# Kernel tuning notes

Measured on AMD Instinct MI355X. Metric: run time of the kernel, lower is better.

Reference implementation:

```python
import jax, jax.numpy as jnp
import numpy as np

FACTOR = 50
IN_CHANNELS = 512

def setup_inputs() -> dict:
    key = jax.random.key(0)
    ks = jax.random.split(key, 9)
    B, Cin, W, H = 16, 256, 64, 64
    D = 512  # out_channels
    L = W * H
    U = FACTOR * int(np.ceil(np.log(L)))  # 450
    return {
        "input_1": jax.random.normal(ks[0], (B, Cin, W, H), jnp.float32),
        "input_2": jax.random.normal(ks[1], (B, Cin, W, H), jnp.float32),
        "Wq": jax.random.normal(ks[2], (D, 2 * Cin), jnp.float32) * 0.02,
        "bq": jax.random.normal(ks[3], (D,), jnp.float32) * 0.02,
        "Wk": jax.random.normal(ks[4], (D, 2 * Cin), jnp.float32) * 0.02,
        "bk": jax.random.normal(ks[5], (D,), jnp.float32) * 0.02,
        "Wv": jax.random.normal(ks[6], (D, 2 * Cin), jnp.float32) * 0.02,
        "bv": jax.random.normal(ks[7], (D,), jnp.float32) * 0.02,
        "idx_sample": jax.random.randint(ks[8], (U,), 0, L, jnp.int32),
    }

def reference(input_1, input_2, Wq, bq, Wk, bk, Wv, bv, idx_sample):
    x = jnp.concatenate([input_1, input_2], axis=1)  # [B, 2*Cin, W, H]
    B, C, Wd, Ht = x.shape
    L = Wd * Ht
    D = Wq.shape[0]
    # 1x1 convs == per-pixel channel matmul; then torch's raw .view to [B,1,L,D]
    def proj(Wm, bm):
        y = jnp.einsum('bchw,oc->bohw', x, Wm) + bm[None, :, None, None]
        return y.reshape(B, 1, L, D)  # memory reinterpretation, as in torch .view
    q = proj(Wq, bq)
    k = proj(Wk, bk)
    v = proj(Wv, bv)

    u = min(FACTOR * int(np.ceil(np.log(L))), L)  # n_top == sample_k here
    # sampled Q-K scores
    K_sample = k[:, :, idx_sample, :]                      # [B,1,U,D]
    QKs = jnp.einsum('bhld,bhsd->bhls', q, K_sample)       # [B,1,L,U]
    M = QKs.max(-1) - QKs.sum(-1) / L                      # sparsity measure [B,1,L]
    M_top = jax.lax.top_k(M, u)[1]                         # [B,1,u]
    Q_reduce = jnp.take_along_axis(q, M_top[..., None], axis=2)  # [B,1,u,D]
    scores = jnp.einsum('bhud,bhld->bhul', Q_reduce, k)    # [B,1,u,L]
    scores = scores * (1.0 / IN_CHANNELS ** 0.5)

    # initial context: mean of V broadcast over queries
    context = jnp.broadcast_to(v.mean(axis=2, keepdims=True), (B, 1, L, D))
    attn = jax.nn.softmax(scores, axis=-1)                 # [B,1,u,L]
    upd = jnp.einsum('bhul,bhld->bhud', attn, v)           # [B,1,u,D]
    bI = jnp.arange(B)[:, None, None]
    hI = jnp.arange(1)[None, :, None]
    context = context.at[bI, hI, M_top].set(upd)
    # transpose(2,1) then torch .view to [B, D, W, H]
    out = context.transpose(0, 2, 1, 3).reshape(B, D, Wd, Ht)
    return out
```

## Files before the change

kernel.cpp:

```cpp
#include <hip/hip_runtime.h>
#include <cstdint>
#include <cstddef>

#define L_DIM 4096
#define D_DIM 512
#define CIN   256
#define BATCH 16
#define KSPLIT 4

typedef _Float16 half8 __attribute__((ext_vector_type(8)));
typedef unsigned short ushort8 __attribute__((ext_vector_type(8)));
typedef float f32x4 __attribute__((ext_vector_type(4)));

__device__ __forceinline__ void gld16(const _Float16* g, _Float16* l) {
    __builtin_amdgcn_global_load_lds(
        (const __attribute__((address_space(1))) unsigned int*)g,
        (__attribute__((address_space(3))) unsigned int*)l,
        16, 0, 0);
}

__global__ __launch_bounds__(256) void convert_w(
    const float* __restrict__ Wq, const float* __restrict__ Wk,
    const float* __restrict__ Wv,
    _Float16* __restrict__ Wh, _Float16* __restrict__ Wl)
{
    const int w = blockIdx.y;
    const float* src = (w == 0) ? Wq : (w == 1) ? Wk : Wv;
    int i = blockIdx.x * 256 + threadIdx.x;
    float xv = src[i];
    _Float16 hi = (_Float16)xv;
    Wh[(size_t)w * 262144 + i] = hi;
    Wl[(size_t)w * 262144 + i] = (_Float16)(xv - (float)hi);
}

__global__ __launch_bounds__(256) void convert_x(
    const float* __restrict__ x1, const float* __restrict__ x2,
    _Float16* __restrict__ XTh, _Float16* __restrict__ XTl, int phase)
{
    const int bb = blockIdx.z;
    const int b = phase * 8 + bb;
    const int s0 = blockIdx.x * 64;
    const int c0 = blockIdx.y * 64;
    __shared__ float t[64][65];
    const int tid = threadIdx.x;
    const int g = tid >> 6, sy = tid & 63;
    const float* src = (c0 < CIN)
        ? (x1 + (size_t)b * CIN * L_DIM + (size_t)c0 * L_DIM)
        : (x2 + (size_t)b * CIN * L_DIM + (size_t)(c0 - CIN) * L_DIM);
    #pragma unroll
    for (int r = 0; r < 16; r++) {
        int cl = g * 16 + r;
        t[cl][sy] = src[(size_t)cl * L_DIM + s0 + sy];
    }
    __syncthreads();
    _Float16* outh = XTh + (size_t)bb * L_DIM * 512 + (size_t)s0 * 512 + c0;
    _Float16* outl = XTl + (size_t)bb * L_DIM * 512 + (size_t)s0 * 512 + c0;
    #pragma unroll
    for (int r = 0; r < 16; r++) {
        int sl = g * 16 + r;
        float xv = t[sy][sl];
        _Float16 hi = (_Float16)xv;
        float lo = xv - (float)hi;
        outh[(size_t)sl * 512 + sy] = hi;
        outl[(size_t)sl * 512 + sy] = (_Float16)lo;
    }
}

__global__ __launch_bounds__(256) void proj_mfma(
    const _Float16* __restrict__ Wh, const _Float16* __restrict__ Wl,
    const _Float16* __restrict__ XTh, const _Float16* __restrict__ XTl,
    const float* __restrict__ bq, const float* __restrict__ bk,
    const float* __restrict__ bv,
    _Float16* __restrict__ qh, _Float16* __restrict__ ql,
    _Float16* __restrict__ kh, _Float16* __restrict__ kl,
    _Float16* __restrict__ vh,
    int phase)
{
    const int z = blockIdx.z;
    const int bb = z / 3, w = z % 3;
    const int b = phase * 8 + bb;
    const _Float16* Ah_g = Wh + (size_t)w * 262144;
    const _Float16* Al_g = Wl + (size_t)w * 262144;
    const _Float16* Bh_g = XTh + (size_t)bb * ((size_t)L_DIM * 512);
    const _Float16* Bl_g = XTl + (size_t)bb * ((size_t)L_DIM * 512);
    const float* bias = (w == 0) ? bq : (w == 1) ? bk : bv;
    _Float16* outh = ((w == 0) ? qh : (w == 1) ? kh : vh) + (size_t)b * ((size_t)D_DIM * L_DIM);
    _Float16* outl = ((w == 0) ? ql : (w == 1) ? kl : (_Float16*)0);
    if (outl) outl += (size_t)b * ((size_t)D_DIM * L_DIM);

    const int m0 = blockIdx.y * 128;
    const int n0 = blockIdx.x * 128;

    __shared__ _Float16 lds[4 * 128 * 32];
    _Float16* ldsA_h = lds;
    _Float16* ldsA_l = lds + 4096;
    _Float16* ldsB_h = lds + 8192;
    _Float16* ldsB_l = lds + 12288;

    const int tid = threadIdx.x;
    const int w4 = tid >> 6, lane = tid & 63;
    const int lr = lane & 15, quad = lane >> 4;
    const int wr = w4 >> 1, wc = w4 & 1;

    f32x4 acc[4][4] = {};

    const int q1 = w4 * 128 + lane, q2 = q1 + 64;
    const int r1 = q1 >> 2, c41 = q1 & 3;
    const int r2 = q2 >> 2, c42 = q2 & 3;

    const _Float16* pAh1 = Ah_g + (size_t)(m0 + r1) * 512 + c41 * 8;
    const _Float16* pAh2 = Ah_g + (size_t)(m0 + r2) * 512 + c42 * 8;
    const _Float16* pAl1 = Al_g + (size_t)(m0 + r1) * 512 + c41 * 8;
    const _Float16* pAl2 = Al_g + (size_t)(m0 + r2) * 512 + c42 * 8;
    const _Float16* pBh1 = Bh_g + (size_t)(n0 + r1) * 512 + c41 * 8;
    const _Float16* pBh2 = Bh_g + (size_t)(n0 + r2) * 512 + c42 * 8;
    const _Float16* pBl1 = Bl_g + (size_t)(n0 + r1) * 512 + c41 * 8;
    const _Float16* pBl2 = Bl_g + (size_t)(n0 + r2) * 512 + c42 * 8;

    _Float16* d1 = (_Float16*)(lds) + (size_t)(w4 * 128) * 8;
    _Float16* d2 = (_Float16*)(lds) + (size_t)(w4 * 128 + 64) * 8;

    for (int k0 = 0; k0 < 512; k0 += 32) {
        if (k0) __syncthreads();
        gld16(pAh1 + k0, d1);
        gld16(pAh2 + k0, d2);
        gld16(pAl1 + k0, d1 + 4096);
        gld16(pAl2 + k0, d2 + 4096);
        gld16(pBh1 + k0, d1 + 8192);
        gld16(pBh2 + k0, d2 + 8192);
        gld16(pBl1 + k0, d1 + 12288);
        gld16(pBl2 + k0, d2 + 12288);
        __syncthreads();

        half8 fAh[4], fAl[4];
        #pragma unroll
        for (int i = 0; i < 4; i++) {
            int m = wr * 64 + i * 16 + lr;
            fAh[i] = *(const half8*)(ldsA_h + m * 32 + quad * 8);
            fAl[i] = *(const half8*)(ldsA_l + m * 32 + quad * 8);
        }
        #pragma unroll
        for (int j = 0; j < 4; j++) {
            int n = wc * 64 + j * 16 + lr;
            half8 fBh = *(const half8*)(ldsB_h + n * 32 + quad * 8);
            half8 fBl = *(const half8*)(ldsB_l + n * 32 + quad * 8);
            #pragma unroll
            for (int i = 0; i < 4; i++) {
                acc[i][j] = __builtin_amdgcn_mfma_f32_16x16x32_f16(fAh[i], fBh, acc[i][j], 0, 0, 0);
                acc[i][j] = __builtin_amdgcn_mfma_f32_16x16x32_f16(fAl[i], fBh, acc[i][j], 0, 0, 0);
                acc[i][j] = __builtin_amdgcn_mfma_f32_16x16x32_f16(fAh[i], fBl, acc[i][j], 0, 0, 0);
            }
        }
    }

    #pragma unroll
    for (int i = 0; i < 4; i++) {
        int mg = m0 + wr * 64 + i * 16 + quad * 4;
        #pragma unroll
        for (int r = 0; r < 4; r++) {
            float bvv = bias[mg + r];
            #pragma unroll
            for (int j = 0; j < 4; j++) {
                int ng = n0 + wc * 64 + j * 16 + lr;
                float val = acc[i][j][r] + bvv;
                _Float16 hi = (_Float16)val;
                size_t off = (size_t)(mg + r) * L_DIM + ng;
                outh[off] = hi;
                if (w != 2) outl[off] = (_Float16)(val - (float)hi);
            }
        }
    }
}

__global__ __launch_bounds__(256) void qks_mfma(
    const _Float16* __restrict__ qh, const _Float16* __restrict__ ql,
    const _Float16* __restrict__ kh, const _Float16* __restrict__ kl,
    const int* __restrict__ idx_sample,
    float* __restrict__ Mmax, float* __restrict__ Msum, int U, int nst)
{
    const int b = blockIdx.z;
    const int stile = blockIdx.y;
    const int l0 = blockIdx.x * 128;
    const int s0 = stile * 128;
    const size_t perB = (size_t)D_DIM * L_DIM;
    const _Float16* qh_b = qh + (size_t)b * perB;
    const _Float16* ql_b = ql + (size_t)b * perB;
    const _Float16* kh_b = kh + (size_t)b * perB;
    const _Float16* kl_b = kl + (size_t)b * perB;

    __shared__ _Float16 ldsAh[4096], ldsAl[4096];
    __shared__ _Float16 ldsBh[4096], ldsBl[4096];
    __shared__ int sidx[128];
    __shared__ float redm[8][128];
    __shared__ float reds[8][128];

    const int tid = threadIdx.x;
    const int w4 = tid >> 6, lane = tid & 63;
    const int lr = lane & 15, quad = lane >> 4;
    const int ws = w4 >> 1, wl = w4 & 1;

    if (tid < 128) {
        int s = s0 + tid;
        sidx[tid] = (s < U) ? idx_sample[s] : idx_sample[0];
    }
    __syncthreads();

    f32x4 acc[4][4] = {};

    for (int k0 = 0; k0 < 512; k0 += 32) {
        #pragma unroll
        for (int t = 0; t < 2; t++) {
            int c = w4 * 128 + t * 64 + lane;
            int row = c >> 2, part = c & 3;
            int krow = sidx[row];
            size_t go = (size_t)krow * 512 + k0 + part * 8;
            size_t qo = (size_t)(l0 + row) * 512 + k0 + part * 8;
            int base = (w4 * 128 + t * 64) * 8;
            gld16(kh_b + go, ldsAh + base);
            gld16(kl_b + go, ldsAl + base);
            gld16(qh_b + qo, ldsBh + base);
            gld16(ql_b + qo, ldsBl + base);
        }
        __syncthreads();

        half8 fAh[4], fAl[4];
        #pragma unroll
        for (int i = 0; i < 4; i++) {
            int s = ws * 64 + i * 16 + lr;
            fAh[i] = *(const half8*)(ldsAh + s * 32 + quad * 8);
            fAl[i] = *(const half8*)(ldsAl + s * 32 + quad * 8);
        }
        #pragma unroll
        for (int j = 0; j < 4; j++) {
            int l = wl * 64 + j * 16 + lr;
            half8 fBh = *(const half8*)(ldsBh + l * 32 + quad * 8);
            half8 fBl = *(const half8*)(ldsBl + l * 32 + quad * 8);
            #pragma unroll
            for (int i = 0; i < 4; i++) {
                acc[i][j] = __builtin_amdgcn_mfma_f32_16x16x32_f16(fAh[i], fBh, acc[i][j], 0, 0, 0);
                acc[i][j] = __builtin_amdgcn_mfma_f32_16x16x32_f16(fAl[i], fBh, acc[i][j], 0, 0, 0);
                acc[i][j] = __builtin_amdgcn_mfma_f32_16x16x32_f16(fAh[i], fBl, acc[i][j], 0, 0, 0);
            }
        }
        __syncthreads();
    }

    float runmax[4], runsum[4];
    #pragma unroll
    for (int j = 0; j < 4; j++) { runmax[j] = -__builtin_inff(); runsum[j] = 0.f; }
    #pragma unroll
    for (int i = 0; i < 4; i++) {
        #pragma unroll
        for (int r = 0; r < 4; r++) {
            int sg = s0 + ws * 64 + i * 16 + quad * 4 + r;
            if (sg < U) {
                #pragma unroll
                for (int j = 0; j < 4; j++) {
                    runmax[j] = fmaxf(runmax[j], acc[i][j][r]);
                    runsum[j] += acc[i][j][r];
                }
            }
        }
    }
    #pragma unroll
    for (int j = 0; j < 4; j++) {
        int l = wl * 64 + j * 16 + lr;
        redm[ws * 4 + quad][l] = runmax[j];
        reds[ws * 4 + quad][l] = runsum[j];
    }
    __syncthreads();
    if (tid < 128) {
        float gm = -__builtin_inff(), gs = 0.f;
        #pragma unroll
        for (int t = 0; t < 8; t++) { gm = fmaxf(gm, redm[t][tid]); gs += reds[t][tid]; }
        size_t o = ((size_t)b * nst + stile) * L_DIM + l0 + tid;
        Mmax[o] = gm;
        Msum[o] = gs;
    }
}

__global__ __launch_bounds__(512) void topk_select(
    const float* __restrict__ Mmax, const float* __restrict__ Msum,
    int* __restrict__ topidx, int U, int nst)
{
    const int b = blockIdx.x;
    const int tid = threadIdx.x;
    __shared__ int wcnt[8];
    __shared__ int basec;

    unsigned mykey[8];
    #pragma unroll
    for (int t = 0; t < 8; t++) {
        int l = t * 512 + tid;
        float gm = -__builtin_inff(), gs = 0.f;
        for (int st = 0; st < nst; st++) {
            size_t o = ((size_t)b * nst + st) * L_DIM + l;
            gm = fmaxf(gm, Mmax[o]);
            gs += Msum[o];
        }
        float M = gm - gs * (1.f / (float)L_DIM);
        unsigned bits = __float_as_uint(M);
        mykey[t] = (bits & 0x80000000u) ? ~bits : (bits | 0x80000000u);
    }
    if (tid == 0) basec = 0;

    const int wv = tid >> 6, lane = tid & 63;
    unsigned lo = 0u, hi = 0xFFFFFFFFu;
    while (lo < hi) {
        unsigned hl = hi - lo;
        unsigned mid = lo + (hl >> 1) + (hl & 1u);
        int c = 0;
        #pragma unroll
        for (int t = 0; t < 8; t++) c += (mykey[t] >= mid) ? 1 : 0;
        #pragma unroll
        for (int o = 32; o > 0; o >>= 1) c += __shfl_down(c, o, 64);
        if (lane == 0) wcnt[wv] = c;
        __syncthreads();
        int total = 0;
        #pragma unroll
        for (int i = 0; i < 8; i++) total += wcnt[i];
        if (total >= U) lo = mid; else hi = mid - 1;
        __syncthreads();
    }
    #pragma unroll
    for (int t = 0; t < 8; t++) {
        if (mykey[t] >= lo) {
            int pos = atomicAdd(&basec, 1);
            if (pos < U) topidx[b * U + pos] = t * 512 + tid;
        }
    }
}

__global__ __launch_bounds__(512) void vmean_partial(
    const _Float16* __restrict__ vh, float* __restrict__ partial)
{
    const int ch = blockIdx.x, b = blockIdx.y;
    const int d = threadIdx.x;
    const _Float16* vhb = vh + (size_t)b * ((size_t)D_DIM * L_DIM);
    float acc = 0.f;
    const int lbeg = ch * 128;
    for (int l = lbeg; l < lbeg + 128; l++)
        acc += (float)vhb[(size_t)l * D_DIM + d];
    partial[((size_t)b * 32 + ch) * D_DIM + d] = acc;
}

__global__ __launch_bounds__(512) void vmean_reduce(const float* __restrict__ partial,
                                                    float* __restrict__ vmean)
{
    const int b = blockIdx.x;
    const int d = threadIdx.x;
    float acc = 0.f;
    for (int ch = 0; ch < 32; ch++) acc += partial[((size_t)b * 32 + ch) * D_DIM + d];
    vmean[b * D_DIM + d] = acc * (1.f / (float)L_DIM);
}

__global__ __launch_bounds__(256) void fill_out(const float* __restrict__ vmean,
                                                float* __restrict__ out)
{
    const int z = blockIdx.x;
    const int b = z >> 6, lch = z & 63;
    __shared__ float vm[512];
    vm[threadIdx.x] = vmean[b * 512 + threadIdx.x];
    vm[threadIdx.x + 256] = vmean[b * 512 + threadIdx.x + 256];
    __syncthreads();
    float* op = out + (size_t)b * ((size_t)D_DIM * L_DIM) + (size_t)lch * 64 * 512;
    #pragma unroll
    for (int it = 0; it < 32; it++) {
        int flat = (threadIdx.x + it * 256) * 4;
        int d = flat & 511;
        float4 r = { vm[d], vm[d + 1], vm[d + 2], vm[d + 3] };
        *(float4*)&op[flat] = r;
    }
}

__global__ __launch_bounds__(256) void zero_sel(const int* __restrict__ topidx,
                                                float* __restrict__ out, int U)
{
    const int u = blockIdx.x, b = blockIdx.y;
    int row = topidx[b * U + u];
    float2 z = { 0.f, 0.f };
    *(float2*)&out[(size_t)b * ((size_t)D_DIM * L_DIM) + (size_t)row * 512
                   + threadIdx.x * 2] = z;
}

__global__ __launch_bounds__(256) void scores_mfma(
    const _Float16* __restrict__ qh, const _Float16* __restrict__ kh,
    const int* __restrict__ topidx,
    _Float16* __restrict__ sh, int U)
{
    const int b = blockIdx.z;
    const int s0 = blockIdx.x * 128;
    const int u0 = blockIdx.y * 128;
    const size_t perB = (size_t)D_DIM * L_DIM;
    const _Float16* qh_b = qh + (size_t)b * perB;
    const _Float16* kh_b = kh + (size_t)b * perB;
    _Float16* sh_b = sh + (size_t)b * (size_t)U * L_DIM;

    __shared__ _Float16 ldsAh[4096];
    __shared__ _Float16 ldsBh[4096];
    __shared__ int arow[128];

    const int tid = threadIdx.x;
    const int w4 = tid >> 6, lane = tid & 63;
    const int lr = lane & 15, quad = lane >> 4;
    const int wu = w4 >> 1, wn = w4 & 1;

    if (tid < 128) {
        int u = u0 + tid;
        arow[tid] = topidx[b * U + (u < U ? u : U - 1)];
    }
    __syncthreads();

    f32x4 acc[4][4] = {};

    for (int k0 = 0; k0 < 512; k0 += 32) {
        #pragma unroll
        for (int t = 0; t < 2; t++) {
            int c = w4 * 128 + t * 64 + lane;
            int row = c >> 2, part = c & 3;
            size_t go = (size_t)arow[row] * 512 + k0 + part * 8;
            size_t ko = (size_t)(s0 + row) * 512 + k0 + part * 8;
            int base = (w4 * 128 + t * 64) * 8;
            gld16(qh_b + go, ldsAh + base);
            gld16(kh_b + ko, ldsBh + base);
        }
        __syncthreads();

        half8 fAh[4];
        #pragma unroll
        for (int i = 0; i < 4; i++) {
            int u = wu * 64 + i * 16 + lr;
            fAh[i] = *(const half8*)(ldsAh + u * 32 + quad * 8);
        }
        #pragma unroll
        for (int j = 0; j < 4; j++) {
            int s = wn * 64 + j * 16 + lr;
            half8 fBh = *(const half8*)(ldsBh + s * 32 + quad * 8);
            #pragma unroll
            for (int i = 0; i < 4; i++)
                acc[i][j] = __builtin_amdgcn_mfma_f32_16x16x32_f16(fAh[i], fBh, acc[i][j], 0, 0, 0);
        }
        __syncthreads();
    }

    const float scale = 0.044194173824159216f;
    #pragma unroll
    for (int i = 0; i < 4; i++) {
        #pragma unroll
        for (int r = 0; r < 4; r++) {
            int u = u0 + wu * 64 + i * 16 + quad * 4 + r;
            if (u < U) {
                #pragma unroll
                for (int j = 0; j < 4; j++) {
                    int s = s0 + wn * 64 + j * 16 + lr;
                    sh_b[(size_t)u * L_DIM + s] = (_Float16)(acc[i][j][r] * scale);
                }
            }
        }
    }
}

__global__ __launch_bounds__(256) void softmax_h(_Float16* __restrict__ sh)
{
    _Float16* hrow = sh + (size_t)blockIdx.x * L_DIM;
    const int tid = threadIdx.x;
    float x[16];
    #pragma unroll
    for (int t = 0; t < 2; t++) {
        half8 h8 = *(const half8*)(hrow + tid * 8 + t * 2048);
        #pragma unroll
        for (int i = 0; i < 8; i++) x[t * 8 + i] = (float)h8[i];
    }
    __shared__ float red[256];
    float lm = -__builtin_inff();
    #pragma unroll
    for (int i = 0; i < 16; i++) lm = fmaxf(lm, x[i]);
    red[tid] = lm;
    __syncthreads();
    for (int o = 128; o > 0; o >>= 1) {
        if (tid < o) red[tid] = fmaxf(red[tid], red[tid + o]);
        __syncthreads();
    }
    float m = red[0];
    __syncthreads();
    float ls = 0.f;
    #pragma unroll
    for (int i = 0; i < 16; i++) { x[i] = __expf(x[i] - m); ls += x[i]; }
    red[tid] = ls;
    __syncthreads();
    for (int o = 128; o > 0; o >>= 1) {
        if (tid < o) red[tid] += red[tid + o];
        __syncthreads();
    }
    float inv = 1.f / red[0];
    #pragma unroll
    for (int t = 0; t < 2; t++) {
        half8 h8;
        #pragma unroll
        for (int i = 0; i < 8; i++) h8[i] = (_Float16)(x[t * 8 + i] * inv);
        *(half8*)(hrow + tid * 8 + t * 2048) = h8;
    }
}

__global__ __launch_bounds__(256) void upd_mfma(
    const _Float16* __restrict__ sh, const _Float16* __restrict__ vh,
    const int* __restrict__ topidx, float* __restrict__ out, int U)
{
    const int zz = blockIdx.z;
    const int b = zz >> 2, ks = zz & 3;
    const int n0 = blockIdx.y * 128;
    const int u0 = blockIdx.x * 128;
    const size_t perB = (size_t)D_DIM * L_DIM;
    const _Float16* ah_b = sh + (size_t)b * (size_t)U * L_DIM;
    const _Float16* vh_b = vh + (size_t)b * perB;

    __shared__ _Float16 ldsAh[4096];
    __shared__ _Float16 ldsBh[4096];

    const int tid = threadIdx.x;
    const int w4 = tid >> 6, lane = tid & 63;
    const int lr = lane & 15, quad = lane >> 4;
    const int wu = w4 >> 1, wd = w4 & 1;

    const int part = tid & 15, spair = tid >> 4;
    const int s_b = spair * 2;
    const int colw = ((spair >> 2) + part) & 3;
    const int so2 = (s_b & 7);

    f32x4 acc[4][4] = {};

    const int kbeg = ks * (L_DIM / KSPLIT);
    const int kend = kbeg + (L_DIM / KSPLIT);
    for (int k0 = kbeg; k0 < kend; k0 += 32) {
        #pragma unroll
        for (int t = 0; t < 2; t++) {
            int c = w4 * 128 + t * 64 + lane;
            int u = c >> 2, pt = c & 3;
            int urow = u0 + u; if (urow >= U) urow = U - 1;
            size_t ao = (size_t)urow * L_DIM + k0 + pt * 8;
            int base = (w4 * 128 + t * 64) * 8;
            gld16(ah_b + ao, ldsAh + base);
        }
        {
            const _Float16* s0p = vh_b + (size_t)(k0 + s_b) * 512 + n0 + part * 8;
            const _Float16* s1p = s0p + 512;
            ushort8 a0 = *(const ushort8*)s0p;
            ushort8 a1 = *(const ushort8*)s1p;
            #pragma unroll
            for (int t = 0; t < 8; t++) {
                int dd = part * 8 + t;
                unsigned int ph = (unsigned int)a0[t] | ((unsigned int)a1[t] << 16);
                *(unsigned int*)(ldsBh + dd * 32 + colw * 8 + so2) = ph;
            }
        }
        __syncthreads();

        half8 fAh[4];
        #pragma unroll
        for (int i = 0; i < 4; i++) {
            int u = wu * 64 + i * 16 + lr;
            fAh[i] = *(const half8*)(ldsAh + u * 32 + quad * 8);
        }
        #pragma unroll
        for (int j = 0; j < 4; j++) {
            int dd = wd * 64 + j * 16 + lr;
            int col = (quad + (dd >> 3)) & 3;
            half8 fBh = *(const half8*)(ldsBh + dd * 32 + col * 8);
            #pragma unroll
            for (int i = 0; i < 4; i++)
                acc[i][j] = __builtin_amdgcn_mfma_f32_16x16x32_f16(fAh[i], fBh, acc[i][j], 0, 0, 0);
        }
        __syncthreads();
    }

    #pragma unroll
    for (int i = 0; i < 4; i++) {
        #pragma unroll
        for (int r = 0; r < 4; r++) {
            int u = u0 + wu * 64 + i * 16 + quad * 4 + r;
            if (u < U) {
                int lrow = topidx[b * U + u];
                #pragma unroll
                for (int j = 0; j < 4; j++) {
                    int dd = n0 + wd * 64 + j * 16 + lr;
                    unsafeAtomicAdd(&out[(size_t)b * perB + (size_t)lrow * 512 + dd],
                                    acc[i][j][r]);
                }
            }
        }
    }
}

extern "C" void kernel_launch(void* const* d_in, const int* in_sizes, int n_in,
                              void* d_out, int out_size, void* d_ws, size_t ws_size,
                              hipStream_t stream)
{
    const float* x1 = (const float*)d_in[0];
    const float* x2 = (const float*)d_in[1];
    const float* Wq = (const float*)d_in[2];
    const float* bq = (const float*)d_in[3];
    const float* Wk = (const float*)d_in[4];
    const float* bk = (const float*)d_in[5];
    const float* Wv = (const float*)d_in[6];
    const float* bv = (const float*)d_in[7];
    const int*  idx = (const int*)d_in[8];
    const int U = in_sizes[8];
    const int nst = (U + 127) / 128;

    float* out = (float*)d_out;

    const size_t perB = (size_t)D_DIM * L_DIM;
    const size_t tenH = (size_t)BATCH * perB;
    _Float16* qh = (_Float16*)d_ws;
    _Float16* ql = qh + tenH;
    _Float16* kh = ql + tenH;
    _Float16* kl = kh + tenH;
    _Float16* vh = kl + tenH;
    float* S = (float*)(vh + tenH);

    _Float16* XTh = (_Float16*)S;
    _Float16* XTl = XTh + (size_t)8 * L_DIM * 512;
    _Float16* Wh  = XTl + (size_t)8 * L_DIM * 512;
    _Float16* Wl  = Wh + (size_t)3 * 512 * 512;

    _Float16* sh = (_Float16*)S;
    float* vmean = (float*)(sh + (size_t)BATCH * (size_t)U * L_DIM);
    float* partU = vmean + (size_t)BATCH * D_DIM;
    float* vpart = partU;
    float* Mmax  = partU;
    float* Msum  = Mmax + (size_t)BATCH * nst * L_DIM;
    int* topidx  = (int*)(partU + (size_t)2 * BATCH * 4 * L_DIM);

    convert_w<<<dim3(1024, 3), 256, 0, stream>>>(Wq, Wk, Wv, Wh, Wl);

    for (int phase = 0; phase < 2; phase++) {
        convert_x<<<dim3(64, 8, 8), 256, 0, stream>>>(x1, x2, XTh, XTl, phase);
        proj_mfma<<<dim3(L_DIM / 128, D_DIM / 128, 8 * 3), 256, 0, stream>>>(
            Wh, Wl, XTh, XTl, bq, bk, bv, qh, ql, kh, kl, vh, phase);
    }

    vmean_partial<<<dim3(32, BATCH), 512, 0, stream>>>(vh, vpart);
    vmean_reduce<<<BATCH, 512, 0, stream>>>(vpart, vmean);
    fill_out<<<BATCH * 64, 256, 0, stream>>>(vmean, out);

    qks_mfma<<<dim3(L_DIM / 128, nst, BATCH), 256, 0, stream>>>(
        qh, ql, kh, kl, idx, Mmax, Msum, U, nst);
    topk_select<<<BATCH, 512, 0, stream>>>(Mmax, Msum, topidx, U, nst);

    const int utiles = (U + 127) / 128;
    scores_mfma<<<dim3(L_DIM / 128, utiles, BATCH), 256, 0, stream>>>(
        qh, kh, topidx, sh, U);
    softmax_h<<<BATCH * U, 256, 0, stream>>>(sh);
    zero_sel<<<dim3(U, BATCH), 256, 0, stream>>>(topidx, out, U);
    upd_mfma<<<dim3(utiles, D_DIM / 128, BATCH * KSPLIT), 256, 0, stream>>>(
        sh, vh, topidx, out, U);
}
```

Before: 915.6 us.

## Swizzle LDS tiles to avoid bank conflicts and split V projection to single-precision path

Applies an XOR swizzle to the 16-byte column chunks in LDS across the projection, QK-sample, scores and update GEMMs, so that MFMA fragment reads from 64-byte rows no longer hit the same banks. It also splits the V projection into its own kernel that skips the low-half (Wl, XTl) operand loads and the two correction MFMAs, since V is stored only in fp16 high. The V kernel therefore uses half the LDS and a third of the MFMAs. In exchange there is one more kernel launch per phase, and V is now computed with less precision than before because the W and X low-half corrections are dropped.

```diff
diff --git a/kernel.cpp b/kernel.cpp
--- a/kernel.cpp
+++ b/kernel.cpp
@@ -66,27 +66,24 @@
     }
 }
 
-__global__ __launch_bounds__(256) void proj_mfma(
+__global__ __launch_bounds__(256) void proj_mfma_qk(
     const _Float16* __restrict__ Wh, const _Float16* __restrict__ Wl,
     const _Float16* __restrict__ XTh, const _Float16* __restrict__ XTl,
     const float* __restrict__ bq, const float* __restrict__ bk,
-    const float* __restrict__ bv,
     _Float16* __restrict__ qh, _Float16* __restrict__ ql,
     _Float16* __restrict__ kh, _Float16* __restrict__ kl,
-    _Float16* __restrict__ vh,
     int phase)
 {
     const int z = blockIdx.z;
-    const int bb = z / 3, w = z % 3;
+    const int bb = z >> 1, w = z & 1;
     const int b = phase * 8 + bb;
     const _Float16* Ah_g = Wh + (size_t)w * 262144;
     const _Float16* Al_g = Wl + (size_t)w * 262144;
     const _Float16* Bh_g = XTh + (size_t)bb * ((size_t)L_DIM * 512);
     const _Float16* Bl_g = XTl + (size_t)bb * ((size_t)L_DIM * 512);
-    const float* bias = (w == 0) ? bq : (w == 1) ? bk : bv;
-    _Float16* outh = ((w == 0) ? qh : (w == 1) ? kh : vh) + (size_t)b * ((size_t)D_DIM * L_DIM);
-    _Float16* outl = ((w == 0) ? ql : (w == 1) ? kl : (_Float16*)0);
-    if (outl) outl += (size_t)b * ((size_t)D_DIM * L_DIM);
+    const float* bias = (w == 0) ? bq : bk;
+    _Float16* outh = ((w == 0) ? qh : kh) + (size_t)b * ((size_t)D_DIM * L_DIM);
+    _Float16* outl = ((w == 0) ? ql : kl) + (size_t)b * ((size_t)D_DIM * L_DIM);
 
     const int m0 = blockIdx.y * 128;
     const int n0 = blockIdx.x * 128;
@@ -105,8 +102,8 @@
     f32x4 acc[4][4] = {};
 
     const int q1 = w4 * 128 + lane, q2 = q1 + 64;
-    const int r1 = q1 >> 2, c41 = q1 & 3;
-    const int r2 = q2 >> 2, c42 = q2 & 3;
+    const int r1 = q1 >> 2, c41 = (q1 & 3) ^ ((r1 >> 1) & 3);
+    const int r2 = q2 >> 2, c42 = (q2 & 3) ^ ((r2 >> 1) & 3);
 
     const _Float16* pAh1 = Ah_g + (size_t)(m0 + r1) * 512 + c41 * 8;
     const _Float16* pAh2 = Ah_g + (size_t)(m0 + r2) * 512 + c42 * 8;
@@ -119,6 +116,8 @@
 
     _Float16* d1 = (_Float16*)(lds) + (size_t)(w4 * 128) * 8;
     _Float16* d2 = (_Float16*)(lds) + (size_t)(w4 * 128 + 64) * 8;
+
+    const int qsw = (quad ^ ((lr >> 1) & 3)) * 8;
 
     for (int k0 = 0; k0 < 512; k0 += 32) {
         if (k0) __syncthreads();
@@ -136,14 +135,14 @@
         #pragma unroll
         for (int i = 0; i < 4; i++) {
             int m = wr * 64 + i * 16 + lr;
-            fAh[i] = *(const half8*)(ldsA_h + m * 32 + quad * 8);
-            fAl[i] = *(const half8*)(ldsA_l + m * 32 + quad * 8);
+            fAh[i] = *(const half8*)(ldsA_h + m * 32 + qsw);
+            fAl[i] = *(const half8*)(ldsA_l + m * 32 + qsw);
         }
         #pragma unroll
         for (int j = 0; j < 4; j++) {
             int n = wc * 64 + j * 16 + lr;
-            half8 fBh = *(const half8*)(ldsB_h + n * 32 + quad * 8);
-            half8 fBl = *(const half8*)(ldsB_l + n * 32 + quad * 8);
+            half8 fBh = *(const half8*)(ldsB_h + n * 32 + qsw);
+            half8 fBl = *(const half8*)(ldsB_l + n * 32 + qsw);
             #pragma unroll
             for (int i = 0; i < 4; i++) {
                 acc[i][j] = __builtin_amdgcn_mfma_f32_16x16x32_f16(fAh[i], fBh, acc[i][j], 0, 0, 0);
@@ -166,7 +165,84 @@
                 _Float16 hi = (_Float16)val;
                 size_t off = (size_t)(mg + r) * L_DIM + ng;
                 outh[off] = hi;
-                if (w != 2) outl[off] = (_Float16)(val - (float)hi);
+                outl[off] = (_Float16)(val - (float)hi);
+            }
+        }
+    }
+}
+
+__global__ __launch_bounds__(256) void proj_mfma_v(
+    const _Float16* __restrict__ Wh, const _Float16* __restrict__ XTh,
+    const float* __restrict__ bv, _Float16* __restrict__ vh, int phase)
+{
+    const int bb = blockIdx.z;
+    const int b = phase * 8 + bb;
+    const _Float16* Ah_g = Wh + (size_t)2 * 262144;
+    const _Float16* Bh_g = XTh + (size_t)bb * ((size_t)L_DIM * 512);
+    _Float16* outh = vh + (size_t)b * ((size_t)D_DIM * L_DIM);
+
+    const int m0 = blockIdx.y * 128;
+    const int n0 = blockIdx.x * 128;
+
+    __shared__ _Float16 lds[2 * 128 * 32];
+    _Float16* ldsA_h = lds;
+    _Float16* ldsB_h = lds + 4096;
+
+    const int tid = threadIdx.x;
+    const int w4 = tid >> 6, lane = tid & 63;
+    const int lr = lane & 15, quad = lane >> 4;
+    const int wr = w4 >> 1, wc = w4 & 1;
+
+    f32x4 acc[4][4] = {};
+
+    const int q1 = w4 * 128 + lane, q2 = q1 + 64;
+    const int r1 = q1 >> 2, c41 = (q1 & 3) ^ ((r1 >> 1) & 3);
+    const int r2 = q2 >> 2, c42 = (q2 & 3) ^ ((r2 >> 1) & 3);
+
+    const _Float16* pAh1 = Ah_g + (size_t)(m0 + r1) * 512 + c41 * 8;
+    const _Float16* pAh2 = Ah_g + (size_t)(m0 + r2) * 512 + c42 * 8;
+    const _Float16* pBh1 = Bh_g + (size_t)(n0 + r1) * 512 + c41 * 8;
+    const _Float16* pBh2 = Bh_g + (size_t)(n0 + r2) * 512 + c42 * 8;
+
+    _Float16* d1 = (_Float16*)(lds) + (size_t)(w4 * 128) * 8;
+    _Float16* d2 = (_Float16*)(lds) + (size_t)(w4 * 128 + 64) * 8;
+
+    const int qsw = (quad ^ ((lr >> 1) & 3)) * 8;
+
+    for (int k0 = 0; k0 < 512; k0 += 32) {
+        if (k0) __syncthreads();
+        gld16(pAh1 + k0, d1);
+        gld16(pAh2 + k0, d2);
+        gld16(pBh1 + k0, d1 + 4096);
+        gld16(pBh2 + k0, d2 + 4096);
+        __syncthreads();
+
+        half8 fAh[4];
+        #pragma unroll
+        for (int i = 0; i < 4; i++) {
+            int m = wr * 64 + i * 16 + lr;
+            fAh[i] = *(const half8*)(ldsA_h + m * 32 + qsw);
+        }
+        #pragma unroll
+        for (int j = 0; j < 4; j++) {
+            int n = wc * 64 + j * 16 + lr;
+            half8 fBh = *(const half8*)(ldsB_h + n * 32 + qsw);
+            #pragma unroll
+            for (int i = 0; i < 4; i++)
+                acc[i][j] = __builtin_amdgcn_mfma_f32_16x16x32_f16(fAh[i], fBh, acc[i][j], 0, 0, 0);
+        }
+    }
+
+    #pragma unroll
+    for (int i = 0; i < 4; i++) {
+        int mg = m0 + wr * 64 + i * 16 + quad * 4;
+        #pragma unroll
+        for (int r = 0; r < 4; r++) {
+            float bvv = bv[mg + r];
+            #pragma unroll
+            for (int j = 0; j < 4; j++) {
+                int ng = n0 + wc * 64 + j * 16 + lr;
+                outh[(size_t)(mg + r) * L_DIM + ng] = (_Float16)(acc[i][j][r] + bvv);
             }
         }
     }
@@ -206,12 +282,13 @@
     __syncthreads();
 
     f32x4 acc[4][4] = {};
+    const int qsw = (quad ^ ((lr >> 1) & 3)) * 8;
 
     for (int k0 = 0; k0 < 512; k0 += 32) {
         #pragma unroll
         for (int t = 0; t < 2; t++) {
             int c = w4 * 128 + t * 64 + lane;
-            int row = c >> 2, part = c & 3;
+            int row = c >> 2, part = (c & 3) ^ ((row >> 1) & 3);
             int krow = sidx[row];
             size_t go = (size_t)krow * 512 + k0 + part * 8;
             size_t qo = (size_t)(l0 + row) * 512 + k0 + part * 8;
@@ -227,14 +304,14 @@
         #pragma unroll
         for (int i = 0; i < 4; i++) {
             int s = ws * 64 + i * 16 + lr;
-            fAh[i] = *(const half8*)(ldsAh + s * 32 + quad * 8);
-            fAl[i] = *(const half8*)(ldsAl + s * 32 + quad * 8);
+            fAh[i] = *(const half8*)(ldsAh + s * 32 + qsw);
+            fAl[i] = *(const half8*)(ldsAl + s * 32 + qsw);
         }
         #pragma unroll
         for (int j = 0; j < 4; j++) {
             int l = wl * 64 + j * 16 + lr;
-            half8 fBh = *(const half8*)(ldsBh + l * 32 + quad * 8);
-            half8 fBl = *(const half8*)(ldsBl + l * 32 + quad * 8);
+            half8 fBh = *(const half8*)(ldsBh + l * 32 + qsw);
+            half8 fBl = *(const half8*)(ldsBl + l * 32 + qsw);
             #pragma unroll
             for (int i = 0; i < 4; i++) {
                 acc[i][j] = __builtin_amdgcn_mfma_f32_16x16x32_f16(fAh[i], fBh, acc[i][j], 0, 0, 0);
@@ -412,12 +489,13 @@
     __syncthreads();
 
     f32x4 acc[4][4] = {};
+    const int qsw = (quad ^ ((lr >> 1) & 3)) * 8;
 
     for (int k0 = 0; k0 < 512; k0 += 32) {
         #pragma unroll
         for (int t = 0; t < 2; t++) {
             int c = w4 * 128 + t * 64 + lane;
-            int row = c >> 2, part = c & 3;
+            int row = c >> 2, part = (c & 3) ^ ((row >> 1) & 3);
             size_t go = (size_t)arow[row] * 512 + k0 + part * 8;
             size_t ko = (size_t)(s0 + row) * 512 + k0 + part * 8;
             int base = (w4 * 128 + t * 64) * 8;
@@ -430,12 +508,12 @@
         #pragma unroll
         for (int i = 0; i < 4; i++) {
             int u = wu * 64 + i * 16 + lr;
-            fAh[i] = *(const half8*)(ldsAh + u * 32 + quad * 8);
+            fAh[i] = *(const half8*)(ldsAh + u * 32 + qsw);
         }
         #pragma unroll
         for (int j = 0; j < 4; j++) {
             int s = wn * 64 + j * 16 + lr;
-            half8 fBh = *(const half8*)(ldsBh + s * 32 + quad * 8);
+            half8 fBh = *(const half8*)(ldsBh + s * 32 + qsw);
             #pragma unroll
             for (int i = 0; i < 4; i++)
                 acc[i][j] = __builtin_amdgcn_mfma_f32_16x16x32_f16(fAh[i], fBh, acc[i][j], 0, 0, 0);
@@ -528,6 +606,7 @@
     const int so2 = (s_b & 7);
 
     f32x4 acc[4][4] = {};
+    const int qsw = (quad ^ ((lr >> 1) & 3)) * 8;
 
     const int kbeg = ks * (L_DIM / KSPLIT);
     const int kend = kbeg + (L_DIM / KSPLIT);
@@ -535,7 +614,7 @@
         #pragma unroll
         for (int t = 0; t < 2; t++) {
             int c = w4 * 128 + t * 64 + lane;
-            int u = c >> 2, pt = c & 3;
+            int u = c >> 2, pt = (c & 3) ^ ((u >> 1) & 3);
             int urow = u0 + u; if (urow >= U) urow = U - 1;
             size_t ao = (size_t)urow * L_DIM + k0 + pt * 8;
             int base = (w4 * 128 + t * 64) * 8;
@@ -559,7 +638,7 @@
         #pragma unroll
         for (int i = 0; i < 4; i++) {
             int u = wu * 64 + i * 16 + lr;
-            fAh[i] = *(const half8*)(ldsAh + u * 32 + quad * 8);
+            fAh[i] = *(const half8*)(ldsAh + u * 32 + qsw);
         }
         #pragma unroll
         for (int j = 0; j < 4; j++) {
@@ -635,8 +714,10 @@
 
     for (int phase = 0; phase < 2; phase++) {
         convert_x<<<dim3(64, 8, 8), 256, 0, stream>>>(x1, x2, XTh, XTl, phase);
-        proj_mfma<<<dim3(L_DIM / 128, D_DIM / 128, 8 * 3), 256, 0, stream>>>(
-            Wh, Wl, XTh, XTl, bq, bk, bv, qh, ql, kh, kl, vh, phase);
+        proj_mfma_qk<<<dim3(L_DIM / 128, D_DIM / 128, 8 * 2), 256, 0, stream>>>(
+            Wh, Wl, XTh, XTl, bq, bk, qh, ql, kh, kl, phase);
+        proj_mfma_v<<<dim3(L_DIM / 128, D_DIM / 128, 8), 256, 0, stream>>>(
+            Wh, XTh, bv, vh, phase);
     }
 
     vmean_partial<<<dim3(32, BATCH), 512, 0, stream>>>(vh, vpart);
```

Measured after the change: 883.8 us, median of 2. 3.5% less time.
